# Performance work log

Hardware: AMD Instinct MI355X
Metric: run time of the kernel (lower is better)

The kernel has to match this reference:

```python
import jax, jax.numpy as jnp
import numpy as np


def setup_inputs() -> dict:
    key = jax.random.key(0)
    k0, k1, k2, k3 = jax.random.split(key, 4)
    B, S, E, D, L = 4, 128, 768, 128, 40
    return {
        "emb0": jax.random.normal(k0, (B, S, E), jnp.float32),
        "emb1": jax.random.normal(k1, (B, S, E), jnp.float32),
        "att": jnp.ones((B, S), dtype=bool),
        "W_arc": jax.random.normal(k2, (D, E), jnp.float32) * 0.05,
        "W_lbl": jax.random.normal(k3, (L, 2 * E), jnp.float32) * 0.05,
    }


def reference(emb0, emb1, att, W_arc, W_lbl):
    B, S, E = emb1.shape
    L = W_lbl.shape[0]
    # --- RootedGraphPredictor: linear transform + all-pairs squared distances ---
    dep = jnp.einsum('bse,de->bsd', emb0, W_arc)                      # [B,S,D]
    diff = dep[:, :, None, :] - dep[:, None, :, :]                    # [B,S,S,D]
    distances = jnp.sum(diff * diff, axis=-1)                         # [B,S,S]
    # log(softmin(distances)) == log_softmax(-distances)
    parent = jax.nn.log_softmax(-distances, axis=-1)                  # [B,S,S]
    # --- DependencyLabelClassifier ---
    # Faithful packing order of emb_sentences_expanded: first S*(S-1) rows are
    # (i,j) pairs in row-major order SKIPPING the diagonal, last S rows are
    # (emb[i], ones). The attention mask, however, is laid out in FULL row-major
    # (j,k) order (index j*S+k) -- this mismatch is in the original code and is
    # reproduced faithfully here.
    p = jnp.arange(S * S)
    tail = p >= S * (S - 1)
    i_comp = p // (S - 1)
    j_raw = p % (S - 1)
    j_comp = j_raw + (j_raw >= i_comp).astype(j_raw.dtype)
    i_idx = jnp.where(tail, p - S * (S - 1), i_comp)
    j_idx = jnp.where(tail, 0, j_comp)
    first = emb1[:, i_idx, :]                                          # [B,S*S,E]
    second = jnp.where(tail[None, :, None], 1.0, emb1[:, j_idx, :])    # [B,S*S,E]
    pair = jnp.concatenate([first, second], axis=-1)                   # [B,S*S,2E]
    mlp_out = jnp.einsum('bpe,le->bpl', pair, W_lbl)                   # [B,S*S,L]
    eye = jnp.eye(S, dtype=bool)
    mask = (att[:, :, None] & att[:, None, :] & ~eye).reshape(B, S * S)
    logits = jnp.where(mask[:, :, None], mlp_out, -jnp.inf)            # [B,S*S,L]
    lbl_logits = jnp.log(logits).reshape(B, S, S, L)                   # log of logits (nan where <=0/-inf)
    lbl_parent = jnp.nan_to_num(lbl_logits + parent[:, :, :, None], nan=-10.0)
    return (dep, distances, lbl_parent)
```

## Files before the change

kernel.cpp:

```cpp
#include <hip/hip_runtime.h>


__device__ __forceinline__ float wsum_f32(float v) {
#pragma unroll
    for (int off = 32; off; off >>= 1) v += __shfl_down(v, off, 64);
    return v;
}
__device__ __forceinline__ double wsum_f64(double v) {
#pragma unroll
    for (int off = 32; off; off >>= 1) v += __shfl_down(v, off, 64);
    return v;
}

__global__ __launch_bounds__(256) void k1_proj(
    const float* __restrict__ emb0,
    const float* __restrict__ emb1,
    const float* __restrict__ W_arc,
    const float* __restrict__ W_lbl,
    float* __restrict__ out_dep,
    double* __restrict__ A1,
    double* __restrict__ A2,
    double* __restrict__ Cd)
{
    const int tid  = threadIdx.x;
    const int lane = tid & 63;
    const int wv   = tid >> 6;
    const int blk  = blockIdx.x;
    const int base = lane * 4;

    if (blk < 256) {
        __shared__ float e0[1536];
        __shared__ float col_out[256];
        const int r0 = blk * 2;
        const float* src = emb0 + r0 * 768;
        for (int idx = tid * 4; idx < 1536; idx += 1024)
            *(float4*)(e0 + idx) = *(const float4*)(src + idx);
        __syncthreads();

        const float4 ea0 = *(const float4*)(e0 + base);
        const float4 ea1 = *(const float4*)(e0 + 256 + base);
        const float4 ea2 = *(const float4*)(e0 + 512 + base);
        const float4 eb0 = *(const float4*)(e0 + 768 + base);
        const float4 eb1 = *(const float4*)(e0 + 1024 + base);
        const float4 eb2 = *(const float4*)(e0 + 1280 + base);

        for (int cc = 0; cc < 32; ++cc) {
            const int c = wv * 32 + cc;
            const float* w = W_arc + c * 768 + base;
            const float4 w0 = *(const float4*)(w);
            const float4 w1 = *(const float4*)(w + 256);
            const float4 w2 = *(const float4*)(w + 512);
            float s0 = w0.x*ea0.x + w0.y*ea0.y + w0.z*ea0.z + w0.w*ea0.w
                     + w1.x*ea1.x + w1.y*ea1.y + w1.z*ea1.z + w1.w*ea1.w
                     + w2.x*ea2.x + w2.y*ea2.y + w2.z*ea2.z + w2.w*ea2.w;
            float s1 = w0.x*eb0.x + w0.y*eb0.y + w0.z*eb0.z + w0.w*eb0.w
                     + w1.x*eb1.x + w1.y*eb1.y + w1.z*eb1.z + w1.w*eb1.w
                     + w2.x*eb2.x + w2.y*eb2.y + w2.z*eb2.z + w2.w*eb2.w;
            s0 = wsum_f32(s0);
            s1 = wsum_f32(s1);
            if (lane == 0) { col_out[c] = s0; col_out[128 + c] = s1; }
        }
        __syncthreads();
        out_dep[r0 * 128 + tid] = col_out[tid];
    } else {
        __shared__ float e1[1536];
        __shared__ double a_out[160];
        const int r0 = (blk - 256) * 2;
        const float* src = emb1 + r0 * 768;
        for (int idx = tid * 4; idx < 1536; idx += 1024)
            *(float4*)(e1 + idx) = *(const float4*)(src + idx);
        __syncthreads();

        const float4 fa0 = *(const float4*)(e1 + base);
        const float4 fa1 = *(const float4*)(e1 + 256 + base);
        const float4 fa2 = *(const float4*)(e1 + 512 + base);
        const float4 fb0 = *(const float4*)(e1 + 768 + base);
        const float4 fb1 = *(const float4*)(e1 + 1024 + base);
        const float4 fb2 = *(const float4*)(e1 + 1280 + base);

        for (int cc = 0; cc < 20; ++cc) {
            const int col  = wv * 20 + cc;
            const int half = col / 40;
            const int l    = col - half * 40;
            const float* w = W_lbl + l * 1536 + half * 768 + base;
            const float4 w0 = *(const float4*)(w);
            const float4 w1 = *(const float4*)(w + 256);
            const float4 w2 = *(const float4*)(w + 512);
            double s0 = (double)w0.x*fa0.x + (double)w0.y*fa0.y + (double)w0.z*fa0.z + (double)w0.w*fa0.w
                      + (double)w1.x*fa1.x + (double)w1.y*fa1.y + (double)w1.z*fa1.z + (double)w1.w*fa1.w
                      + (double)w2.x*fa2.x + (double)w2.y*fa2.y + (double)w2.z*fa2.z + (double)w2.w*fa2.w;
            double s1 = (double)w0.x*fb0.x + (double)w0.y*fb0.y + (double)w0.z*fb0.z + (double)w0.w*fb0.w
                      + (double)w1.x*fb1.x + (double)w1.y*fb1.y + (double)w1.z*fb1.z + (double)w1.w*fb1.w
                      + (double)w2.x*fb2.x + (double)w2.y*fb2.y + (double)w2.z*fb2.z + (double)w2.w*fb2.w;
            s0 = wsum_f64(s0);
            s1 = wsum_f64(s1);
            if (lane == 0) { a_out[col] = s0; a_out[80 + col] = s1; }
        }
        __syncthreads();
        if (tid < 160) {
            const int row = tid / 80, rem = tid - row * 80;
            const int half = rem / 40, l = rem - half * 40;
            double* dst = half ? A2 : A1;
            dst[(r0 + row) * 40 + l] = a_out[row * 80 + rem];
        }
        if (blk == 256) {
            for (int cc = 0; cc < 10; ++cc) {
                const int l = wv * 10 + cc;
                const float* w = W_lbl + l * 1536 + 768 + base;
                const float4 w0 = *(const float4*)(w);
                const float4 w1 = *(const float4*)(w + 256);
                const float4 w2 = *(const float4*)(w + 512);
                double s = (double)w0.x + (double)w0.y + (double)w0.z + (double)w0.w
                         + (double)w1.x + (double)w1.y + (double)w1.z + (double)w1.w
                         + (double)w2.x + (double)w2.y + (double)w2.z + (double)w2.w;
                s = wsum_f64(s);
                if (lane == 0) Cd[l] = s;
            }
        }
    }
}

__global__ __launch_bounds__(256) void k2_rows(
    const float* __restrict__ dep,
    const double* __restrict__ A1,
    const double* __restrict__ A2,
    const double* __restrict__ Cd,
    float* __restrict__ out_dist,
    float* __restrict__ out_lbl)
{
    __shared__ double Aloc[5120];
    __shared__ double a1loc[80];
    __shared__ float depi[128];
    __shared__ float dists[128];
    __shared__ float partial[256];
    __shared__ float red[4];
    __shared__ float lse_sh;

    const int tid = threadIdx.x;
    const int bi = blockIdx.x;
    const int b = bi >> 7;
    const int i = bi & 127;
    const bool last = (i == 127);
    const float* depb = dep + b * 16384;

    const double* asrc = (last ? A1 : A2) + b * 5120;
    for (int t = tid; t < 5120; t += 256) Aloc[t] = asrc[t];
    if (!last) {
        if (tid < 80) a1loc[tid] = A1[b * 5120 + i * 40 + tid];
    } else {
        if (tid < 40) a1loc[tid] = Cd[tid];
    }
    if (tid < 128) depi[tid] = depb[i * 128 + tid];
    __syncthreads();

    {
        const int j = tid & 127, h = tid >> 7;
        const float* dj = depb + j * 128 + h * 64;
        const float* di = depi + h * 64;
        float acc = 0.f;
        for (int d = 0; d < 64; d += 4) {
            float4 v = *(const float4*)(dj + d);
            float d0 = v.x - di[d + 0];
            float d1 = v.y - di[d + 1];
            float d2 = v.z - di[d + 2];
            float d3 = v.w - di[d + 3];
            acc += d0 * d0 + d1 * d1 + d2 * d2 + d3 * d3;
        }
        partial[tid] = acc;
    }
    __syncthreads();
    float ex = 0.f;
    if (tid < 128) {
        const float d = partial[tid] + partial[tid + 128];
        dists[tid] = d;
        out_dist[bi * 128 + tid] = d;
        ex = expf(-d);
    }
    float s = wsum_f32(ex);
    if ((tid & 63) == 0) red[tid >> 6] = s;
    __syncthreads();
    if (tid == 0) lse_sh = logf(red[0] + red[1] + red[2] + red[3]);
    __syncthreads();

    const float lse = lse_sh;
    float* outrow = out_lbl + bi * 5120;

    if (!last) {
        for (int k = 0; k < 5; ++k) {
            const int idx = k * 1024 + tid * 4;
            float4 o;
            float* oc = &o.x;
#pragma unroll
            for (int e = 0; e < 4; ++e) {
                const int id = idx + e;
                const int j = id / 40;
                const int l = id - j * 40;
                float r;
                if (j == i) {
                    r = -10.0f;
                } else {
                    const int s2 = i + j;
                    const int carry = (s2 >= 127) ? 1 : 0;
                    const int jr = s2 - 127 * carry;
                    const int jm = jr + ((jr >= i + carry) ? 1 : 0);
                    const double v = a1loc[carry * 40 + l] + Aloc[jm * 40 + l];
                    r = (v > 0.0) ? (logf((float)v) - dists[j] - lse)
                      : ((v < 0.0) ? -10.0f : -3.4028234663852886e+38f);
                }
                oc[e] = r;
            }
            *(float4*)(outrow + idx) = o;
        }
    } else {
        for (int k = 0; k < 5; ++k) {
            const int idx = k * 1024 + tid * 4;
            float4 o;
            float* oc = &o.x;
#pragma unroll
            for (int e = 0; e < 4; ++e) {
                const int id = idx + e;
                const int j = id / 40;
                const int l = id - j * 40;
                float r;
                if (j == i) {
                    r = -10.0f;
                } else {
                    const double v = Aloc[j * 40 + l] + a1loc[l];
                    r = (v > 0.0) ? (logf((float)v) - dists[j] - lse)
                      : ((v < 0.0) ? -10.0f : -3.4028234663852886e+38f);
                }
                oc[e] = r;
            }
            *(float4*)(outrow + idx) = o;
        }
    }
}

extern "C" void kernel_launch(void* const* d_in, const int* in_sizes, int n_in,
                              void* d_out, int out_size, void* d_ws, size_t ws_size,
                              hipStream_t stream)
{
    const float* emb0  = (const float*)d_in[0];
    const float* emb1  = (const float*)d_in[1];
    const float* W_arc = (const float*)d_in[3];
    const float* W_lbl = (const float*)d_in[4];

    float* out      = (float*)d_out;
    float* out_dep  = out;
    float* out_dist = out + 65536;
    float* out_lbl  = out + 131072;

    char* ws = (char*)d_ws;
    double* A1 = (double*)(ws);
    double* A2 = (double*)(ws + 163840);
    double* Cd = (double*)(ws + 327680);

    hipLaunchKernelGGL(k1_proj, dim3(512), dim3(256), 0, stream,
                       emb0, emb1, W_arc, W_lbl, out_dep, A1, A2, Cd);
    hipLaunchKernelGGL(k2_rows, dim3(512), dim3(256), 0, stream,
                       out_dep, A1, A2, Cd, out_dist, out_lbl);
}
```

Baseline: 99.56 us.

## Fuse projection and row kernels into one cooperative kernel with grid sync

Merges the projection kernel and the per-row distance/label kernel into a single cooperative launch. A grid-wide barrier sits between the two phases, and shared memory is overlaid through a union. This removes one kernel launch and the inter-kernel gap. In exchange it adds the cost of a grid sync and requires all 512 blocks to be co-resident, which holds easily on this device.

```diff
diff --git a/kernel.cpp b/kernel.cpp
--- a/kernel.cpp
+++ b/kernel.cpp
@@ -1,4 +1,7 @@
 #include <hip/hip_runtime.h>
+#include <hip/hip_cooperative_groups.h>
+
+namespace cg = cooperative_groups;
 
 
 __device__ __forceinline__ float wsum_f32(float v) {
@@ -12,16 +15,33 @@
     return v;
 }
 
-__global__ __launch_bounds__(256) void k1_proj(
+union SharedU {
+    struct { float e[1536]; float col_out[256]; } p1d;
+    struct { float e[1536]; double a_out[160]; } p1a;
+    struct {
+        double Aloc[5120];
+        double a1loc[80];
+        float depi[128];
+        float dists[128];
+        float partial[256];
+        float red[4];
+        float lse;
+    } p2;
+};
+
+__global__ __launch_bounds__(256, 2) void fused_all(
     const float* __restrict__ emb0,
     const float* __restrict__ emb1,
     const float* __restrict__ W_arc,
     const float* __restrict__ W_lbl,
     float* __restrict__ out_dep,
+    float* __restrict__ out_dist,
+    float* __restrict__ out_lbl,
     double* __restrict__ A1,
     double* __restrict__ A2,
     double* __restrict__ Cd)
 {
+    __shared__ SharedU sh;
     const int tid  = threadIdx.x;
     const int lane = tid & 63;
     const int wv   = tid >> 6;
@@ -29,8 +49,8 @@
     const int base = lane * 4;
 
     if (blk < 256) {
-        __shared__ float e0[1536];
-        __shared__ float col_out[256];
+        float* e0 = sh.p1d.e;
+        float* col_out = sh.p1d.col_out;
         const int r0 = blk * 2;
         const float* src = emb0 + r0 * 768;
         for (int idx = tid * 4; idx < 1536; idx += 1024)
@@ -63,8 +83,8 @@
         __syncthreads();
         out_dep[r0 * 128 + tid] = col_out[tid];
     } else {
-        __shared__ float e1[1536];
-        __shared__ double a_out[160];
+        float* e1 = sh.p1a.e;
+        double* a_out = sh.p1a.a_out;
         const int r0 = (blk - 256) * 2;
         const float* src = emb1 + r0 * 768;
         for (int idx = tid * 4; idx < 1536; idx += 1024)
@@ -118,45 +138,29 @@
             }
         }
     }
-}
-
-__global__ __launch_bounds__(256) void k2_rows(
-    const float* __restrict__ dep,
-    const double* __restrict__ A1,
-    const double* __restrict__ A2,
-    const double* __restrict__ Cd,
-    float* __restrict__ out_dist,
-    float* __restrict__ out_lbl)
-{
-    __shared__ double Aloc[5120];
-    __shared__ double a1loc[80];
-    __shared__ float depi[128];
-    __shared__ float dists[128];
-    __shared__ float partial[256];
-    __shared__ float red[4];
-    __shared__ float lse_sh;
-
-    const int tid = threadIdx.x;
-    const int bi = blockIdx.x;
+
+    cg::this_grid().sync();
+
+    const int bi = blk;
     const int b = bi >> 7;
     const int i = bi & 127;
     const bool last = (i == 127);
-    const float* depb = dep + b * 16384;
+    const float* depb = out_dep + b * 16384;
 
     const double* asrc = (last ? A1 : A2) + b * 5120;
-    for (int t = tid; t < 5120; t += 256) Aloc[t] = asrc[t];
+    for (int t = tid; t < 5120; t += 256) sh.p2.Aloc[t] = asrc[t];
     if (!last) {
-        if (tid < 80) a1loc[tid] = A1[b * 5120 + i * 40 + tid];
+        if (tid < 80) sh.p2.a1loc[tid] = A1[b * 5120 + i * 40 + tid];
     } else {
-        if (tid < 40) a1loc[tid] = Cd[tid];
-    }
-    if (tid < 128) depi[tid] = depb[i * 128 + tid];
+        if (tid < 40) sh.p2.a1loc[tid] = Cd[tid];
+    }
+    if (tid < 128) sh.p2.depi[tid] = depb[i * 128 + tid];
     __syncthreads();
 
     {
         const int j = tid & 127, h = tid >> 7;
         const float* dj = depb + j * 128 + h * 64;
-        const float* di = depi + h * 64;
+        const float* di = sh.p2.depi + h * 64;
         float acc = 0.f;
         for (int d = 0; d < 64; d += 4) {
             float4 v = *(const float4*)(dj + d);
@@ -166,23 +170,23 @@
             float d3 = v.w - di[d + 3];
             acc += d0 * d0 + d1 * d1 + d2 * d2 + d3 * d3;
         }
-        partial[tid] = acc;
+        sh.p2.partial[tid] = acc;
     }
     __syncthreads();
     float ex = 0.f;
     if (tid < 128) {
-        const float d = partial[tid] + partial[tid + 128];
-        dists[tid] = d;
+        const float d = sh.p2.partial[tid] + sh.p2.partial[tid + 128];
+        sh.p2.dists[tid] = d;
         out_dist[bi * 128 + tid] = d;
         ex = expf(-d);
     }
     float s = wsum_f32(ex);
-    if ((tid & 63) == 0) red[tid >> 6] = s;
-    __syncthreads();
-    if (tid == 0) lse_sh = logf(red[0] + red[1] + red[2] + red[3]);
-    __syncthreads();
-
-    const float lse = lse_sh;
+    if ((tid & 63) == 0) sh.p2.red[tid >> 6] = s;
+    __syncthreads();
+    if (tid == 0) sh.p2.lse = logf(sh.p2.red[0] + sh.p2.red[1] + sh.p2.red[2] + sh.p2.red[3]);
+    __syncthreads();
+
+    const float lse = sh.p2.lse;
     float* outrow = out_lbl + bi * 5120;
 
     if (!last) {
@@ -203,8 +207,8 @@
                     const int carry = (s2 >= 127) ? 1 : 0;
                     const int jr = s2 - 127 * carry;
                     const int jm = jr + ((jr >= i + carry) ? 1 : 0);
-                    const double v = a1loc[carry * 40 + l] + Aloc[jm * 40 + l];
-                    r = (v > 0.0) ? (logf((float)v) - dists[j] - lse)
+                    const double v = sh.p2.a1loc[carry * 40 + l] + sh.p2.Aloc[jm * 40 + l];
+                    r = (v > 0.0) ? (logf((float)v) - sh.p2.dists[j] - lse)
                       : ((v < 0.0) ? -10.0f : -3.4028234663852886e+38f);
                 }
                 oc[e] = r;
@@ -225,8 +229,8 @@
                 if (j == i) {
                     r = -10.0f;
                 } else {
-                    const double v = Aloc[j * 40 + l] + a1loc[l];
-                    r = (v > 0.0) ? (logf((float)v) - dists[j] - lse)
+                    const double v = sh.p2.Aloc[j * 40 + l] + sh.p2.a1loc[l];
+                    r = (v > 0.0) ? (logf((float)v) - sh.p2.dists[j] - lse)
                       : ((v < 0.0) ? -10.0f : -3.4028234663852886e+38f);
                 }
                 oc[e] = r;
@@ -255,8 +259,9 @@
     double* A2 = (double*)(ws + 163840);
     double* Cd = (double*)(ws + 327680);
 
-    hipLaunchKernelGGL(k1_proj, dim3(512), dim3(256), 0, stream,
-                       emb0, emb1, W_arc, W_lbl, out_dep, A1, A2, Cd);
-    hipLaunchKernelGGL(k2_rows, dim3(512), dim3(256), 0, stream,
-                       out_dep, A1, A2, Cd, out_dist, out_lbl);
-}
+    void* args[] = { (void*)&emb0, (void*)&emb1, (void*)&W_arc, (void*)&W_lbl,
+                     (void*)&out_dep, (void*)&out_dist, (void*)&out_lbl,
+                     (void*)&A1, (void*)&A2, (void*)&Cd };
+    hipLaunchCooperativeKernel((const void*)fused_all, dim3(512), dim3(256),
+                               args, 0, stream);
+}
```

Measured after the change: 168.4 us. +69.1%, slower.
